# Kernel optimization log

Measured on AMD Instinct MI355X. Metric: run time of the kernel, lower is better.

Reference implementation:

```python
import jax, jax.numpy as jnp
import numpy as np

NUM_HEADS = 16
HEAD_DIM = 80  # embed_dim 1280 / 16


def setup_inputs() -> dict:
    key = jax.random.key(0)
    ks = jax.random.split(key, 5)
    E = NUM_HEADS * HEAD_DIM
    sq, b = 1024, 8
    x = jax.random.normal(ks[0], (sq, b, E), dtype=jnp.float32)
    w_in = jax.random.normal(ks[1], (E, 3 * E), dtype=jnp.float32) * (E ** -0.5)
    b_in = jax.random.normal(ks[2], (3 * E,), dtype=jnp.float32) * 0.01
    w_out = jax.random.normal(ks[3], (E, E), dtype=jnp.float32) * (E ** -0.5)
    b_out = jax.random.normal(ks[4], (E,), dtype=jnp.float32) * 0.01
    return {"x": x, "w_in": w_in, "b_in": b_in, "w_out": w_out, "b_out": b_out}


def reference(x, w_in, b_in, w_out, b_out):
    sq, b, E = x.shape
    H, D = NUM_HEADS, HEAD_DIM
    norm_factor = jnp.asarray(D ** 0.5, x.dtype)
    # in_proj: [sq, b, 3E] -> [sq, b, H, 3D], split into q/k/v along last dim
    mixed = (x @ w_in + b_in).reshape(sq, b, H, 3 * D)
    q, k, v = jnp.split(mixed, 3, axis=-1)  # each [sq, b, H, D]
    # merge (b, H) and move to batch-of-bmm layout [b*H, sq, D]
    q = q.reshape(sq, b * H, D).transpose(1, 0, 2) / norm_factor
    k = k.reshape(sq, b * H, D).transpose(1, 0, 2)
    v = v.reshape(sq, b * H, D).transpose(1, 0, 2)
    scores = jnp.einsum('nqd,nkd->nqk', q, k)  # [b*H, sq, sq]
    probs = jax.nn.softmax(scores, axis=-1)
    ctx = jnp.einsum('nqk,nkd->nqd', probs, v)  # [b*H, sq, D]
    # [b, H, sq, D] -> [sq, b, H, D] -> [sq, b, E]
    ctx = ctx.reshape(b, H, sq, D).transpose(2, 0, 1, 3).reshape(sq, b, E)
    return ctx @ w_out + b_out
```

## Files before the change

kernel.cpp:

```cpp
#include <hip/hip_runtime.h>

#define DEVI __device__ __forceinline__

typedef _Float16 f16x8 __attribute__((ext_vector_type(8)));
typedef _Float16 f16x4v __attribute__((ext_vector_type(4)));
typedef _Float16 f16x2 __attribute__((ext_vector_type(2)));
typedef __fp16 fp16x2 __attribute__((ext_vector_type(2)));
typedef float f32x4 __attribute__((ext_vector_type(4)));
typedef float f32x16 __attribute__((ext_vector_type(16)));

DEVI void gl16(const void* g, void* l) {
  __builtin_amdgcn_global_load_lds((const __attribute__((address_space(1))) void*)g,
                                   (__attribute__((address_space(3))) void*)l, 16, 0, 0);
}

#define VMCNT(N) asm volatile("s_waitcnt vmcnt(" #N ")" ::: "memory")
#define LGKM0() asm volatile("s_waitcnt lgkmcnt(0)" ::: "memory")
#define BARRIER() asm volatile("s_barrier" ::: "memory")

DEVI unsigned pk2(float a, float b) {
  fp16x2 t = __builtin_amdgcn_cvt_pkrtz(a, b);
  return __builtin_bit_cast(unsigned, t);
}

__global__ __launch_bounds__(256) void k_cvt(const float* __restrict__ in, _Float16* __restrict__ out, int n4) {
  int i = blockIdx.x * 256 + threadIdx.x;
  int stride = gridDim.x * 256;
  for (; i < n4; i += stride) {
    float4 v = ((const float4*)in)[i];
    f16x4v h = { (_Float16)v.x, (_Float16)v.y, (_Float16)v.z, (_Float16)v.w };
    ((f16x4v*)out)[i] = h;
  }
}

__global__ __launch_bounds__(256) void k_transpose(const float* __restrict__ in, _Float16* __restrict__ out,
                                                   int R, int C) {
  __shared__ float t[32][33];
  int cb = blockIdx.x * 32, rb = blockIdx.y * 32;
  int tx = threadIdx.x & 31, ty = threadIdx.x >> 5;
  #pragma unroll
  for (int i = ty; i < 32; i += 8) t[i][tx] = in[(size_t)(rb + i) * C + cb + tx];
  __syncthreads();
  #pragma unroll
  for (int i = ty; i < 32; i += 8) out[(size_t)(cb + i) * R + rb + tx] = (_Float16)t[tx][i];
}


#define MM(NLO, AF, BF) do {                                                                       \
    __builtin_amdgcn_s_setprio(1);                                                                 \
    _Pragma("unroll")                                                                              \
    for (int m_ = 0; m_ < 8; m_++) {                                                               \
      acc[m_][NLO]     = __builtin_amdgcn_mfma_f32_16x16x32_f16(AF[m_], BF[NLO],     acc[m_][NLO],     0, 0, 0); \
      acc[m_][NLO + 1] = __builtin_amdgcn_mfma_f32_16x16x32_f16(AF[m_], BF[NLO + 1], acc[m_][NLO + 1], 0, 0, 0); \
    }                                                                                              \
    __builtin_amdgcn_s_setprio(0);                                                                 \
  } while (0)

#define LDA(KT, KK, DST) do {                                                                      \
    const _Float16* bas_ = &smem[(size_t)((((KT) & 1) * 2) + wr) * 8192];                          \
    _Pragma("unroll")                                                                              \
    for (int m_ = 0; m_ < 8; m_++)                                                                 \
      DST[m_] = *(const f16x8*)&bas_[(m_ * 16 + ln) * 64 + (((((KK) * 4) + g) ^ chB) << 3)];       \
  } while (0)

#define LDB(KT, KK, DST) do {                                                                      \
    const _Float16* bas_ = &smem[32768 + (size_t)((((KT) & 1) * 2) + (wc >> 1)) * 8192];           \
    _Pragma("unroll")                                                                              \
    for (int n_ = 0; n_ < 4; n_++)                                                                 \
      DST[n_] = *(const f16x8*)&bas_[((wc & 1) * 64 + n_ * 16 + ln) * 64 + (((((KK) * 4) + g) ^ chB) << 3)]; \
  } while (0)

template<int M, int N, int K>
__global__ __launch_bounds__(512, 2) void k_gemm8(const _Float16* __restrict__ A, const _Float16* __restrict__ BT,
                                                  const float* __restrict__ bias,
                                                  _Float16* __restrict__ qo, _Float16* __restrict__ ko,
                                                  _Float16* __restrict__ vo) {
  extern __shared__ _Float16 smem[];
  constexpr int NT = K / 64;
  constexpr int NI = NT / 2;
  const int tid = threadIdx.x;
  const int w = tid >> 6, lane = tid & 63, ln = lane & 15, g = lane >> 4;
  const int wr = w >> 2, wc = w & 3;
  const int l8 = lane >> 3, l7 = lane & 7;
  const int stChunk = (l7 ^ l8) << 3;
  const int chB = ln & 7;

  constexpr int MT = M / 256;
  const int xcd = blockIdx.x & 7;
  const int i = blockIdx.x >> 3;
  const int bm0 = (xcd * (MT / 8) + (i & 3)) * 256;
  const int bn0 = (i >> 2) * 256;

  auto stgA = [&](int kt, int hh) {
    _Float16* ldsb = &smem[(size_t)((kt & 1) * 2 + hh) * 8192 + w * 1024];
    const _Float16* g0 = &A[(size_t)(bm0 + hh * 128 + w * 16 + l8) * K + kt * 64 + stChunk];
    gl16(g0, ldsb);
    gl16(g0 + (size_t)8 * K, ldsb + 512);
  };
  auto stgB = [&](int kt, int hh) {
    _Float16* ldsb = &smem[32768 + (size_t)((kt & 1) * 2 + hh) * 8192 + w * 1024];
    const _Float16* g0 = &BT[(size_t)(bn0 + hh * 128 + w * 16 + l8) * K + kt * 64 + stChunk];
    gl16(g0, ldsb);
    gl16(g0 + (size_t)8 * K, ldsb + 512);
  };

  f32x4 acc[8][4] = {};
  f16x8 a0[8], a1[8], b0[4], b1[4];

  stgB(0, 0); stgB(0, 1); stgA(0, 0); stgA(0, 1);
  stgB(1, 0); stgB(1, 1); stgA(1, 0);
  VMCNT(6);
  BARRIER();
  LDA(0, 0, a0); LDB(0, 0, b0);

  for (int it = 0; it < NI; ++it) {
    const int T0 = 2 * it, T1 = 2 * it + 1;
    const int S0 = (T0 + 2 < NT) ? T0 + 2 : 0;
    const int S1 = (T1 + 2 < NT) ? T1 + 2 : 1;
    LDB(T0, 1, b1);
    stgA(T1, 1);
    BARRIER();
    MM(0, a0, b0);
    LGKM0(); BARRIER();
    LDA(T0, 1, a1);
    stgB(S0, 0);
    BARRIER();
    MM(2, a0, b0);
    LGKM0(); BARRIER();
    stgB(S0, 1);
    BARRIER();
    MM(0, a1, b1);
    VMCNT(4);
    LGKM0(); BARRIER();
    LDA(T1, 0, a0); LDB(T1, 0, b0);
    stgA(S0, 0);
    BARRIER();
    MM(2, a1, b1);
    LGKM0(); BARRIER();
    LDB(T1, 1, b1);
    stgA(S0, 1);
    BARRIER();
    MM(0, a0, b0);
    LGKM0(); BARRIER();
    LDA(T1, 1, a1);
    stgB(S1, 0);
    BARRIER();
    MM(2, a0, b0);
    LGKM0(); BARRIER();
    stgB(S1, 1);
    BARRIER();
    MM(0, a1, b1);
    VMCNT(4);
    LGKM0(); BARRIER();
    LDA(S0, 0, a0); LDB(S0, 0, b0);
    stgA(S1, 0);
    BARRIER();
    MM(2, a1, b1);
    LGKM0(); BARRIER();
  }

  VMCNT(0);
  BARRIER();
  _Float16* sH = smem;
  #pragma unroll
  for (int n = 0; n < 4; n++) {
    int col = wc * 64 + n * 16 + ln;
    int gcol = bn0 + col;
    float bv = bias[gcol];
    int hq = gcol / 240;
    int tt = gcol - hq * 240;
    float scl = (tt < 80) ? (0.11180339887498948f * 1.4426950408889634f) : 1.0f;
    #pragma unroll
    for (int m = 0; m < 8; m++) {
      #pragma unroll
      for (int r = 0; r < 4; r++) {
        int row = wr * 128 + m * 16 + 4 * g + r;
        sH[row * 256 + col] = (_Float16)((acc[m][n][r] + bv) * scl);
      }
    }
  }
  LGKM0();
  BARRIER();
  #pragma unroll
  for (int i2 = 0; i2 < 16; i2++) {
    int id = tid + 512 * i2;
    int row = id >> 5, c8 = id & 31;
    f16x8 v = *(const f16x8*)&sH[row * 256 + c8 * 8];
    int gcol = bn0 + c8 * 8;
    int grow = bm0 + row;
    int hq = gcol / 240;
    int tt = gcol - hq * 240;
    int reg = tt / 80;
    int cc = tt - reg * 80;
    int s = grow >> 3;
    int head = (grow & 7) * 16 + hq;
    _Float16* dst = (reg == 0) ? qo : (reg == 1) ? ko : vo;
    *(f16x8*)&dst[(size_t)(head * 1024 + s) * 80 + cc] = v;
  }
}

template<int M, int N, int K>
__global__ __launch_bounds__(256) void k_gemm(const _Float16* __restrict__ A, const _Float16* __restrict__ BT,
                                              const float* __restrict__ bias, float* __restrict__ outF) {
  __shared__ _Float16 Al[128 * 32];
  __shared__ _Float16 Bl[128 * 32];
  const int tid = threadIdx.x;
  const int w = tid >> 6, lane = tid & 63, ln = lane & 15, g = lane >> 4;
  const int bm0 = blockIdx.x * 128, bn0 = blockIdx.y * 128;
  const int wm = (w >> 1) * 64, wn = (w & 1) * 64;
  const int r0 = tid >> 2, c0 = (tid & 3) * 8;
  f32x4 acc[4][4] = {};
  for (int kt = 0; kt < K; kt += 32) {
    __syncthreads();
    gl16(&A[(size_t)(bm0 + r0) * K + kt + c0],      &Al[(w * 64) * 8]);
    gl16(&A[(size_t)(bm0 + r0 + 64) * K + kt + c0], &Al[(256 + w * 64) * 8]);
    gl16(&BT[(size_t)(bn0 + r0) * K + kt + c0],      &Bl[(w * 64) * 8]);
    gl16(&BT[(size_t)(bn0 + r0 + 64) * K + kt + c0], &Bl[(256 + w * 64) * 8]);
    __syncthreads();
    f16x8 af[4], bf[4];
    #pragma unroll
    for (int i = 0; i < 4; i++) af[i] = *(const f16x8*)&Al[(wm + i * 16 + ln) * 32 + g * 8];
    #pragma unroll
    for (int i = 0; i < 4; i++) bf[i] = *(const f16x8*)&Bl[(wn + i * 16 + ln) * 32 + g * 8];
    #pragma unroll
    for (int i = 0; i < 4; i++)
      #pragma unroll
      for (int j = 0; j < 4; j++)
        acc[i][j] = __builtin_amdgcn_mfma_f32_16x16x32_f16(af[i], bf[j], acc[i][j], 0, 0, 0);
  }
  #pragma unroll
  for (int j = 0; j < 4; j++) {
    int col = bn0 + wn + j * 16 + ln;
    float bv = bias[col];
    #pragma unroll
    for (int i = 0; i < 4; i++) {
      int mb = bm0 + wm + i * 16 + 4 * g;
      #pragma unroll
      for (int r = 0; r < 4; r++)
        outF[(size_t)(mb + r) * N + col] = acc[i][j][r] + bv;
    }
  }
}

__global__ __launch_bounds__(256) void k_vtrans(const _Float16* __restrict__ vb, _Float16* __restrict__ vT) {
  __shared__ _Float16 t[64][81];
  int head = blockIdx.x >> 4;
  int sb = (blockIdx.x & 15) * 64;
  for (int idx = threadIdx.x; idx < 64 * 80; idx += 256) {
    int s = idx / 80, d = idx - s * 80;
    t[s][d] = vb[(head * 1024 + sb + s) * 80 + d];
  }
  __syncthreads();
  for (int idx = threadIdx.x; idx < 80 * 64; idx += 256) {
    int d = idx >> 6, s = idx & 63;
    vT[(head * 80 + d) * 1024 + sb + s] = t[s][d];
  }
}

__global__ __launch_bounds__(512, 4) void k_attn(const _Float16* __restrict__ qb, const _Float16* __restrict__ kb,
                                                 const _Float16* __restrict__ vT, _Float16* __restrict__ ctxg) {
  extern __shared__ _Float16 smem[];
  _Float16* Kb  = smem;
  _Float16* Vb0 = smem + 5632;
  _Float16* Vb1 = smem + 5632 + 5760;
  _Float16* Pb  = smem + 5632 + 11520;

  const int tid = threadIdx.x;
  const int w = tid >> 6, lane = tid & 63;
  const int ln = lane & 15, g = (lane >> 4) & 3;
  const int l32 = lane & 31, h = lane >> 5;
  const int xcd = blockIdx.x & 7;
  const int j = blockIdx.x >> 3;
  const int head = xcd + 8 * (j & 15);
  const int s0 = (j >> 4) * 256;
  const int bb = head >> 4, h16 = head & 15;

  const int kc1 = (tid < 128) ? tid + 512 : tid;
  const int kr0 = tid / 10, kh0 = tid - kr0 * 10;
  const int kr1 = kc1 / 10, kh1 = kc1 - kr1 * 10;
  const int vr0 = tid >> 3, vh0 = tid & 7;
  const int vr1 = kc1 >> 3, vh1 = kc1 & 7;
  const size_t kbase = (size_t)head * 1024 * 80;
  const size_t vbase = (size_t)head * 80 * 1024;

  uint4 krA, krB, vrA, vrB;
  auto issue = [&](int kt) {
    const _Float16* kg = kb + kbase + (size_t)(kt * 64) * 80;
    krA = *(const uint4*)(kg + kr0 * 80 + kh0 * 8);
    krB = *(const uint4*)(kg + kr1 * 80 + kh1 * 8);
    const _Float16* vg = vT + vbase + kt * 64;
    vrA = *(const uint4*)(vg + (size_t)vr0 * 1024 + vh0 * 8);
    vrB = *(const uint4*)(vg + (size_t)vr1 * 1024 + vh1 * 8);
  };
  auto stage = [&](int kt) {
    *(uint4*)(Kb + kr0 * 88 + kh0 * 8) = krA;
    *(uint4*)(Kb + kr1 * 88 + kh1 * 8) = krB;
    _Float16* vd = (kt & 1) ? Vb1 : Vb0;
    *(uint4*)(vd + vr0 * 72 + vh0 * 8) = vrA;
    *(uint4*)(vd + vr1 * 72 + vh1 * 8) = vrB;
  };

  const int qrow = s0 + w * 32 + l32;
  f16x8 qf[5];
  #pragma unroll
  for (int s = 0; s < 5; s++)
    qf[s] = *(const f16x8*)&qb[(size_t)(head * 1024 + qrow) * 80 + s * 16 + h * 8];

  f32x4 ctxa[2][5] = {};
  float m_run = -INFINITY, l_run = 0.f;

  issue(0);
  stage(0);
  LGKM0();
  BARRIER();
  issue(1);

  for (int kt = 0; kt < 16; ++kt) {
    f32x16 sc[2] = {};
    __builtin_amdgcn_s_setprio(1);
    #pragma unroll
    for (int t = 0; t < 2; ++t)
      #pragma unroll
      for (int s = 0; s < 5; ++s) {
        f16x8 kf = *(const f16x8*)&Kb[(t * 32 + l32) * 88 + s * 16 + h * 8];
        sc[t] = __builtin_amdgcn_mfma_f32_32x32x16_f16(kf, qf[s], sc[t], 0, 0, 0);
      }
    __builtin_amdgcn_s_setprio(0);
    BARRIER();

    float tm = -INFINITY;
    #pragma unroll
    for (int t = 0; t < 2; ++t)
      #pragma unroll
      for (int r = 0; r < 16; ++r) tm = fmaxf(tm, sc[t][r]);
    tm = fmaxf(tm, __shfl_xor(tm, 32));
    float mnew = fmaxf(m_run, tm);
    float fac = exp2f(m_run - mnew);
    float ps = 0.f;
    const int prow = (w * 32 + l32) * 88;
    #pragma unroll
    for (int t = 0; t < 2; ++t)
      #pragma unroll
      for (int rq = 0; rq < 4; ++rq) {
        float p0 = exp2f(sc[t][rq * 4 + 0] - mnew);
        float p1 = exp2f(sc[t][rq * 4 + 1] - mnew);
        float p2 = exp2f(sc[t][rq * 4 + 2] - mnew);
        float p3 = exp2f(sc[t][rq * 4 + 3] - mnew);
        ps += (p0 + p1) + (p2 + p3);
        unsigned long long u = (unsigned long long)pk2(p0, p1) | ((unsigned long long)pk2(p2, p3) << 32);
        *(unsigned long long*)&Pb[prow + t * 32 + rq * 8 + h * 4] = u;
      }
    ps += __shfl_xor(ps, 32);
    l_run = l_run * fac + ps;
    m_run = mnew;
    #pragma unroll
    for (int rb = 0; rb < 2; ++rb)
      #pragma unroll
      for (int r = 0; r < 4; ++r) {
        float fr = __shfl(fac, rb * 16 + 4 * g + r);
        #pragma unroll
        for (int nt = 0; nt < 5; ++nt) ctxa[rb][nt][r] *= fr;
      }
    LGKM0();

    {
      const _Float16* vcur = (kt & 1) ? Vb1 : Vb0;
      __builtin_amdgcn_s_setprio(1);
      #pragma unroll
      for (int kb4 = 0; kb4 < 2; ++kb4) {
        f16x8 pf0 = *(const f16x8*)&Pb[(w * 32 + ln) * 88 + kb4 * 32 + g * 8];
        f16x8 pf1 = *(const f16x8*)&Pb[(w * 32 + 16 + ln) * 88 + kb4 * 32 + g * 8];
        #pragma unroll
        for (int nt = 0; nt < 5; ++nt) {
          f16x8 vf = *(const f16x8*)&vcur[(nt * 16 + ln) * 72 + kb4 * 32 + g * 8];
          ctxa[0][nt] = __builtin_amdgcn_mfma_f32_16x16x32_f16(pf0, vf, ctxa[0][nt], 0, 0, 0);
          ctxa[1][nt] = __builtin_amdgcn_mfma_f32_16x16x32_f16(pf1, vf, ctxa[1][nt], 0, 0, 0);
        }
      }
      __builtin_amdgcn_s_setprio(0);
    }

    stage(kt + 1);
    LGKM0();
    BARRIER();
    issue(kt + 2 < 16 ? kt + 2 : 15);
  }

  #pragma unroll
  for (int rb = 0; rb < 2; ++rb)
    #pragma unroll
    for (int r = 0; r < 4; ++r) {
      float lr = __shfl(l_run, rb * 16 + 4 * g + r);
      float inv = 1.f / lr;
      int s = s0 + w * 32 + rb * 16 + 4 * g + r;
      int base = (s * 8 + bb) * 1280 + h16 * 80;
      #pragma unroll
      for (int nt = 0; nt < 5; ++nt)
        ctxg[base + nt * 16 + ln] = (_Float16)(ctxa[rb][nt][r] * inv);
    }
}

extern "C" void kernel_launch(void* const* d_in, const int* in_sizes, int n_in,
                              void* d_out, int out_size, void* d_ws, size_t ws_size,
                              hipStream_t stream) {
  const float* x     = (const float*)d_in[0];
  const float* w_in  = (const float*)d_in[1];
  const float* b_in  = (const float*)d_in[2];
  const float* w_out = (const float*)d_in[3];
  const float* b_out = (const float*)d_in[4];
  float* out = (float*)d_out;

  char* ws = (char*)d_ws;
  size_t off = 0;
  auto carve = [&](size_t bytes) -> void* {
    void* p = ws + off;
    off += (bytes + 255) & ~(size_t)255;
    return p;
  };
  _Float16* xb     = (_Float16*)carve(8192ull * 1280 * 2);
  _Float16* w_inT  = (_Float16*)carve(3840ull * 1280 * 2);
  _Float16* w_outT = (_Float16*)carve(1280ull * 1280 * 2);
  _Float16* qb     = (_Float16*)carve(128ull * 1024 * 80 * 2);
  _Float16* kbuf   = (_Float16*)carve(128ull * 1024 * 80 * 2);
  _Float16* vb     = (_Float16*)carve(128ull * 1024 * 80 * 2);
  _Float16* vT     = (_Float16*)carve(128ull * 1024 * 80 * 2);
  _Float16* ctxg   = (_Float16*)carve(8192ull * 1280 * 2);
  if (off > ws_size) return;

  hipFuncSetAttribute(reinterpret_cast<const void*>(&k_gemm8<8192, 3840, 1280>),
                      hipFuncAttributeMaxDynamicSharedMemorySize, 131072);
  hipFuncSetAttribute(reinterpret_cast<const void*>(&k_attn),
                      hipFuncAttributeMaxDynamicSharedMemorySize, 79360);

  k_cvt<<<2048, 256, 0, stream>>>(x, xb, 8192 * 1280 / 4);
  k_transpose<<<dim3(120, 40), 256, 0, stream>>>(w_in, w_inT, 1280, 3840);
  k_transpose<<<dim3(40, 40), 256, 0, stream>>>(w_out, w_outT, 1280, 1280);

  k_gemm8<8192, 3840, 1280><<<480, 512, 131072, stream>>>(xb, w_inT, b_in, qb, kbuf, vb);
  k_vtrans<<<2048, 256, 0, stream>>>(vb, vT);
  k_attn<<<512, 512, 79360, stream>>>(qb, kbuf, vT, ctxg);
  k_gemm<8192, 1280, 1280><<<dim3(64, 10), 256, 0, stream>>>(ctxg, w_outT, b_out, out);
}
```

Before: 266.9 us.

## Keep softmax probabilities in registers via permlane32 swap and swizzle K/V LDS tiles

The attention kernel no longer writes P to shared memory and reads it back. The probabilities are packed to fp16 and rearranged across lane halves with v_permlane32_swap, so they feed 32x32x16 MFMAs directly as the B operand, with V^T as the A operand. K is now double-buffered in LDS like V, both tiles use an XOR swizzle instead of padding, and one barrier per iteration is removed. Output stores become 4-wide vectors. The change lowers LDS traffic and synchronisation, but it raises register use, and launch bounds are relaxed from 4 to 2 blocks per CU.

```diff
diff --git a/kernel.cpp b/kernel.cpp
--- a/kernel.cpp
+++ b/kernel.cpp
@@ -8,6 +8,7 @@
 typedef __fp16 fp16x2 __attribute__((ext_vector_type(2)));
 typedef float f32x4 __attribute__((ext_vector_type(4)));
 typedef float f32x16 __attribute__((ext_vector_type(16)));
+typedef unsigned u32x4 __attribute__((ext_vector_type(4)));
 
 DEVI void gl16(const void* g, void* l) {
   __builtin_amdgcn_global_load_lds((const __attribute__((address_space(1))) void*)g,
@@ -21,6 +22,9 @@
 DEVI unsigned pk2(float a, float b) {
   fp16x2 t = __builtin_amdgcn_cvt_pkrtz(a, b);
   return __builtin_bit_cast(unsigned, t);
+}
+DEVI void pl32swap(unsigned &a, unsigned &b) {
+  asm volatile("v_permlane32_swap_b32 %0, %1" : "+v"(a), "+v"(b));
 }
 
 __global__ __launch_bounds__(256) void k_cvt(const float* __restrict__ in, _Float16* __restrict__ out, int n4) {
@@ -257,47 +261,52 @@
   }
 }
 
-__global__ __launch_bounds__(512, 4) void k_attn(const _Float16* __restrict__ qb, const _Float16* __restrict__ kb,
+__global__ __launch_bounds__(512, 2) void k_attn(const _Float16* __restrict__ qb, const _Float16* __restrict__ kb,
                                                  const _Float16* __restrict__ vT, _Float16* __restrict__ ctxg) {
   extern __shared__ _Float16 smem[];
-  _Float16* Kb  = smem;
-  _Float16* Vb0 = smem + 5632;
-  _Float16* Vb1 = smem + 5632 + 5760;
-  _Float16* Pb  = smem + 5632 + 11520;
+  _Float16* Kb0 = smem;
+  _Float16* Kb1 = smem + 8192;
+  _Float16* Vb0 = smem + 16384;
+  _Float16* Vb1 = smem + 16384 + 6144;
 
   const int tid = threadIdx.x;
   const int w = tid >> 6, lane = tid & 63;
-  const int ln = lane & 15, g = (lane >> 4) & 3;
   const int l32 = lane & 31, h = lane >> 5;
+  const int lx = l32 & 7;
   const int xcd = blockIdx.x & 7;
   const int j = blockIdx.x >> 3;
   const int head = xcd + 8 * (j & 15);
   const int s0 = (j >> 4) * 256;
   const int bb = head >> 4, h16 = head & 15;
 
-  const int kc1 = (tid < 128) ? tid + 512 : tid;
+  const int c1 = (tid < 128) ? tid + 512 : tid;
   const int kr0 = tid / 10, kh0 = tid - kr0 * 10;
-  const int kr1 = kc1 / 10, kh1 = kc1 - kr1 * 10;
+  const int kr1 = c1 / 10,  kh1 = c1 - kr1 * 10;
   const int vr0 = tid >> 3, vh0 = tid & 7;
-  const int vr1 = kc1 >> 3, vh1 = kc1 & 7;
-  const size_t kbase = (size_t)head * 1024 * 80;
-  const size_t vbase = (size_t)head * 80 * 1024;
+  const int vr1 = c1 >> 3,  vh1 = c1 & 7;
+  const int kO0 = kr0 * 128 + ((kh0 ^ (kr0 & 7)) << 3);
+  const int kO1 = kr1 * 128 + ((kh1 ^ (kr1 & 7)) << 3);
+  const int vO0 = vr0 * 64 + ((vh0 ^ (vr0 & 7)) << 3);
+  const int vO1 = vr1 * 64 + ((vh1 ^ (vr1 & 7)) << 3);
+  const _Float16* kG0 = kb + (size_t)head * 81920 + kr0 * 80 + kh0 * 8;
+  const _Float16* kG1 = kb + (size_t)head * 81920 + kr1 * 80 + kh1 * 8;
+  const _Float16* vG0 = vT + (size_t)head * 81920 + vr0 * 1024 + vh0 * 8;
+  const _Float16* vG1 = vT + (size_t)head * 81920 + vr1 * 1024 + vh1 * 8;
 
   uint4 krA, krB, vrA, vrB;
   auto issue = [&](int kt) {
-    const _Float16* kg = kb + kbase + (size_t)(kt * 64) * 80;
-    krA = *(const uint4*)(kg + kr0 * 80 + kh0 * 8);
-    krB = *(const uint4*)(kg + kr1 * 80 + kh1 * 8);
-    const _Float16* vg = vT + vbase + kt * 64;
-    vrA = *(const uint4*)(vg + (size_t)vr0 * 1024 + vh0 * 8);
-    vrB = *(const uint4*)(vg + (size_t)vr1 * 1024 + vh1 * 8);
+    krA = *(const uint4*)(kG0 + kt * 5120);
+    krB = *(const uint4*)(kG1 + kt * 5120);
+    vrA = *(const uint4*)(vG0 + kt * 64);
+    vrB = *(const uint4*)(vG1 + kt * 64);
   };
-  auto stage = [&](int kt) {
-    *(uint4*)(Kb + kr0 * 88 + kh0 * 8) = krA;
-    *(uint4*)(Kb + kr1 * 88 + kh1 * 8) = krB;
-    _Float16* vd = (kt & 1) ? Vb1 : Vb0;
-    *(uint4*)(vd + vr0 * 72 + vh0 * 8) = vrA;
-    *(uint4*)(vd + vr1 * 72 + vh1 * 8) = vrB;
+  auto stage = [&](int b) {
+    _Float16* kd = b ? Kb1 : Kb0;
+    _Float16* vd = b ? Vb1 : Vb0;
+    *(uint4*)(kd + kO0) = krA;
+    *(uint4*)(kd + kO1) = krB;
+    *(uint4*)(vd + vO0) = vrA;
+    *(uint4*)(vd + vO1) = vrB;
   };
 
   const int qrow = s0 + w * 32 + l32;
@@ -306,7 +315,7 @@
   for (int s = 0; s < 5; s++)
     qf[s] = *(const f16x8*)&qb[(size_t)(head * 1024 + qrow) * 80 + s * 16 + h * 8];
 
-  f32x4 ctxa[2][5] = {};
+  f32x16 ct[3] = {};
   float m_run = -INFINITY, l_run = 0.f;
 
   issue(0);
@@ -316,87 +325,95 @@
   issue(1);
 
   for (int kt = 0; kt < 16; ++kt) {
-    f32x16 sc[2] = {};
+    const _Float16* kc = (kt & 1) ? Kb1 : Kb0;
+    const _Float16* vc = (kt & 1) ? Vb1 : Vb0;
+
+    f32x16 sc0 = {}, sc1 = {};
     __builtin_amdgcn_s_setprio(1);
     #pragma unroll
-    for (int t = 0; t < 2; ++t)
-      #pragma unroll
-      for (int s = 0; s < 5; ++s) {
-        f16x8 kf = *(const f16x8*)&Kb[(t * 32 + l32) * 88 + s * 16 + h * 8];
-        sc[t] = __builtin_amdgcn_mfma_f32_32x32x16_f16(kf, qf[s], sc[t], 0, 0, 0);
-      }
+    for (int s = 0; s < 5; ++s) {
+      f16x8 kf0 = *(const f16x8*)&kc[l32 * 128 + (((2 * s + h) ^ lx) << 3)];
+      f16x8 kf1 = *(const f16x8*)&kc[(32 + l32) * 128 + (((2 * s + h) ^ lx) << 3)];
+      sc0 = __builtin_amdgcn_mfma_f32_32x32x16_f16(kf0, qf[s], sc0, 0, 0, 0);
+      sc1 = __builtin_amdgcn_mfma_f32_32x32x16_f16(kf1, qf[s], sc1, 0, 0, 0);
+    }
     __builtin_amdgcn_s_setprio(0);
-    BARRIER();
-
-    float tm = -INFINITY;
-    #pragma unroll
-    for (int t = 0; t < 2; ++t)
-      #pragma unroll
-      for (int r = 0; r < 16; ++r) tm = fmaxf(tm, sc[t][r]);
+
+    float mx[8];
+    #pragma unroll
+    for (int i = 0; i < 8; ++i)
+      mx[i] = fmaxf(fmaxf(sc0[i], sc0[i + 8]), fmaxf(sc1[i], sc1[i + 8]));
+    #pragma unroll
+    for (int i = 0; i < 4; ++i) mx[i] = fmaxf(mx[i], mx[i + 4]);
+    float tm = fmaxf(fmaxf(mx[0], mx[2]), fmaxf(mx[1], mx[3]));
     tm = fmaxf(tm, __shfl_xor(tm, 32));
     float mnew = fmaxf(m_run, tm);
     float fac = exp2f(m_run - mnew);
+    float p0[16], p1[16];
+    #pragma unroll
+    for (int i = 0; i < 16; ++i) p0[i] = exp2f(sc0[i] - mnew);
+    #pragma unroll
+    for (int i = 0; i < 16; ++i) p1[i] = exp2f(sc1[i] - mnew);
     float ps = 0.f;
-    const int prow = (w * 32 + l32) * 88;
-    #pragma unroll
-    for (int t = 0; t < 2; ++t)
+    #pragma unroll
+    for (int i = 0; i < 16; ++i) ps += p0[i] + p1[i];
+
+    unsigned fr[4][4];
+    #define PACK4(T, PP) do {                                                \
+        _Pragma("unroll")                                                    \
+        for (int s16 = 0; s16 < 2; ++s16) {                                  \
+          unsigned u0 = pk2(PP[8 * s16 + 0], PP[8 * s16 + 1]);               \
+          unsigned u1 = pk2(PP[8 * s16 + 2], PP[8 * s16 + 3]);               \
+          unsigned u2 = pk2(PP[8 * s16 + 4], PP[8 * s16 + 5]);               \
+          unsigned u3 = pk2(PP[8 * s16 + 6], PP[8 * s16 + 7]);               \
+          pl32swap(u0, u2); pl32swap(u1, u3);                                \
+          fr[2 * (T) + s16][0] = u0; fr[2 * (T) + s16][1] = u1;              \
+          fr[2 * (T) + s16][2] = u2; fr[2 * (T) + s16][3] = u3;              \
+        }                                                                    \
+      } while (0)
+    PACK4(0, p0);
+    PACK4(1, p1);
+
+    l_run = l_run * fac + (ps + __shfl_xor(ps, 32));
+    m_run = mnew;
+
+    #pragma unroll
+    for (int dt = 0; dt < 3; ++dt)
       #pragma unroll
-      for (int rq = 0; rq < 4; ++rq) {
-        float p0 = exp2f(sc[t][rq * 4 + 0] - mnew);
-        float p1 = exp2f(sc[t][rq * 4 + 1] - mnew);
-        float p2 = exp2f(sc[t][rq * 4 + 2] - mnew);
-        float p3 = exp2f(sc[t][rq * 4 + 3] - mnew);
-        ps += (p0 + p1) + (p2 + p3);
-        unsigned long long u = (unsigned long long)pk2(p0, p1) | ((unsigned long long)pk2(p2, p3) << 32);
-        *(unsigned long long*)&Pb[prow + t * 32 + rq * 8 + h * 4] = u;
+      for (int i = 0; i < 16; ++i) ct[dt][i] *= fac;
+
+    __builtin_amdgcn_s_setprio(1);
+    #pragma unroll
+    for (int ss = 0; ss < 4; ++ss) {
+      u32x4 fu = { fr[ss][0], fr[ss][1], fr[ss][2], fr[ss][3] };
+      f16x8 pf = __builtin_bit_cast(f16x8, fu);
+      #pragma unroll
+      for (int dt = 0; dt < 3; ++dt) {
+        f16x8 vf = *(const f16x8*)&vc[(dt * 32 + l32) * 64 + (((2 * ss + h) ^ lx) << 3)];
+        ct[dt] = __builtin_amdgcn_mfma_f32_32x32x16_f16(vf, pf, ct[dt], 0, 0, 0);
       }
-    ps += __shfl_xor(ps, 32);
-    l_run = l_run * fac + ps;
-    m_run = mnew;
-    #pragma unroll
-    for (int rb = 0; rb < 2; ++rb)
-      #pragma unroll
-      for (int r = 0; r < 4; ++r) {
-        float fr = __shfl(fac, rb * 16 + 4 * g + r);
-        #pragma unroll
-        for (int nt = 0; nt < 5; ++nt) ctxa[rb][nt][r] *= fr;
-      }
-    LGKM0();
-
-    {
-      const _Float16* vcur = (kt & 1) ? Vb1 : Vb0;
-      __builtin_amdgcn_s_setprio(1);
-      #pragma unroll
-      for (int kb4 = 0; kb4 < 2; ++kb4) {
-        f16x8 pf0 = *(const f16x8*)&Pb[(w * 32 + ln) * 88 + kb4 * 32 + g * 8];
-        f16x8 pf1 = *(const f16x8*)&Pb[(w * 32 + 16 + ln) * 88 + kb4 * 32 + g * 8];
-        #pragma unroll
-        for (int nt = 0; nt < 5; ++nt) {
-          f16x8 vf = *(const f16x8*)&vcur[(nt * 16 + ln) * 72 + kb4 * 32 + g * 8];
-          ctxa[0][nt] = __builtin_amdgcn_mfma_f32_16x16x32_f16(pf0, vf, ctxa[0][nt], 0, 0, 0);
-          ctxa[1][nt] = __builtin_amdgcn_mfma_f32_16x16x32_f16(pf1, vf, ctxa[1][nt], 0, 0, 0);
-        }
-      }
-      __builtin_amdgcn_s_setprio(0);
-    }
-
-    stage(kt + 1);
-    LGKM0();
-    BARRIER();
-    issue(kt + 2 < 16 ? kt + 2 : 15);
-  }
-
-  #pragma unroll
-  for (int rb = 0; rb < 2; ++rb)
-    #pragma unroll
-    for (int r = 0; r < 4; ++r) {
-      float lr = __shfl(l_run, rb * 16 + 4 * g + r);
-      float inv = 1.f / lr;
-      int s = s0 + w * 32 + rb * 16 + 4 * g + r;
-      int base = (s * 8 + bb) * 1280 + h16 * 80;
-      #pragma unroll
-      for (int nt = 0; nt < 5; ++nt)
-        ctxg[base + nt * 16 + ln] = (_Float16)(ctxa[rb][nt][r] * inv);
+    }
+    __builtin_amdgcn_s_setprio(0);
+
+    if (kt < 15) {
+      stage((kt + 1) & 1);
+      LGKM0();
+      BARRIER();
+      if (kt < 14) issue(kt + 2);
+    }
+  }
+
+  float inv = 1.f / l_run;
+  int sq = s0 + w * 32 + l32;
+  _Float16* outp = ctxg + (size_t)(sq * 8 + bb) * 1280 + h16 * 80 + 4 * h;
+  #pragma unroll
+  for (int dt = 0; dt < 3; ++dt)
+    #pragma unroll
+    for (int rq = 0; rq < 4; ++rq) {
+      if (dt == 2 && rq >= 2) continue;
+      f16x4v o = { (_Float16)(ct[dt][rq * 4 + 0] * inv), (_Float16)(ct[dt][rq * 4 + 1] * inv),
+                   (_Float16)(ct[dt][rq * 4 + 2] * inv), (_Float16)(ct[dt][rq * 4 + 3] * inv) };
+      *(f16x4v*)&outp[dt * 32 + rq * 8] = o;
     }
 }
 
@@ -430,7 +447,7 @@
   hipFuncSetAttribute(reinterpret_cast<const void*>(&k_gemm8<8192, 3840, 1280>),
                       hipFuncAttributeMaxDynamicSharedMemorySize, 131072);
   hipFuncSetAttribute(reinterpret_cast<const void*>(&k_attn),
-                      hipFuncAttributeMaxDynamicSharedMemorySize, 79360);
+                      hipFuncAttributeMaxDynamicSharedMemorySize, 57344);
 
   k_cvt<<<2048, 256, 0, stream>>>(x, xb, 8192 * 1280 / 4);
   k_transpose<<<dim3(120, 40), 256, 0, stream>>>(w_in, w_inT, 1280, 3840);
@@ -438,6 +455,6 @@
 
   k_gemm8<8192, 3840, 1280><<<480, 512, 131072, stream>>>(xb, w_inT, b_in, qb, kbuf, vb);
   k_vtrans<<<2048, 256, 0, stream>>>(vb, vT);
-  k_attn<<<512, 512, 79360, stream>>>(qb, kbuf, vT, ctxg);
+  k_attn<<<512, 512, 57344, stream>>>(qb, kbuf, vT, ctxg);
   k_gemm<8192, 1280, 1280><<<dim3(64, 10), 256, 0, stream>>>(ctxg, w_outT, b_out, out);
 }
```

Result: faster. 255.7 us (-4.2%).
